# Kernel optimization log

Hardware: AMD Instinct MI355X
Metric: run time of the kernel (lower is better)

Reference implementation:

```python
import jax, jax.numpy as jnp
from jax import lax
import numpy as np

BLOCK_SIZE = 11   # cv2 blockSize (odd)
CONSTANT = 2.0    # cv2 C
MAXVAL = 255.0


def _box_mean(x, k):
    """Local k x k mean with BORDER_REPLICATE, matching cv2 ADAPTIVE_THRESH_MEAN_C.
    x: [N,H,W,1] float32. Separable 1-D box filters for efficiency."""
    pad = k // 2
    xp = jnp.pad(x, ((0, 0), (pad, pad), (pad, pad), (0, 0)), mode='edge')
    kh = jnp.full((k, 1, 1, 1), 1.0 / k, dtype=x.dtype)  # HWIO
    kw = jnp.full((1, k, 1, 1), 1.0 / k, dtype=x.dtype)
    dn = ('NHWC', 'HWIO', 'NHWC')
    y = lax.conv_general_dilated(xp, kh, (1, 1), 'VALID', dimension_numbers=dn)
    y = lax.conv_general_dilated(y, kw, (1, 1), 'VALID', dimension_numbers=dn)
    return y  # [N,H,W,1]


def setup_inputs() -> dict:
    key = jax.random.key(0)
    # grayscale pixel intensities in [0, 255]
    x = jax.random.uniform(key, (128, 512, 512, 1), dtype=jnp.float32) * 255.0
    return {"x": x}


def reference(x):
    # cv2.adaptiveThreshold(..., ADAPTIVE_THRESH_MEAN_C, THRESH_BINARY_INV, blockSize, C):
    #   T(x,y) = mean_{kxk}(src) - C
    #   dst = 0 if src > T else maxValue
    thresh = _box_mean(x, BLOCK_SIZE) - CONSTANT
    out = jnp.where(x > thresh, jnp.float32(0.0), jnp.float32(MAXVAL))
    return out
```

## Files before the change

kernel.cpp:

```cpp
#include <hip/hip_runtime.h>


constexpr int W   = 512;
constexpr int H   = 512;
constexpr int PAD = 5;
constexpr int KS  = 11;
constexpr int TPB = 256;
constexpr int RPB = 32;
constexpr int WP  = W + 2 * PAD;

__global__ __launch_bounds__(TPB, 8)
void AdaptiveThresholding_57904749085171_kernel(const float* __restrict__ x,
                                                float* __restrict__ out)
{
    __shared__ float mv[2][WP];

    const int t  = (int)threadIdx.x;
    const int c0 = 2 * t;
    const int y0 = (int)blockIdx.x * RPB;
    const size_t ioff = (size_t)blockIdx.y * (size_t)(W * H);
    const float* __restrict__ xi = x + ioff;
    float* __restrict__ oi = out + ioff;
    const float wv = (float)(1.0 / 11.0);

    float r0[KS], r1[KS];

    #pragma unroll
    for (int k = 0; k < KS - 1; ++k) {
        int j = y0 - PAD + k;
        int src = j < 0 ? 0 : (j >= H ? H - 1 : j);
        const float2 v = *(const float2*)(xi + (size_t)src * W + c0);
        r0[k] = v.x; r1[k] = v.y;
    }
    float p0, p1;
    {
        int j = y0 + PAD;
        int src = j >= H ? H - 1 : j;
        const float2 v = *(const float2*)(xi + (size_t)src * W + c0);
        p0 = v.x; p1 = v.y;
    }

    for (int y = y0; y < y0 + RPB; ++y) {
        r0[KS - 1] = p0;
        r1[KS - 1] = p1;

        float a0 = 0.0f, a1 = 0.0f;
        #pragma unroll
        for (int d = 0; d < KS; ++d) {
            a0 = fmaf(r0[d], wv, a0);
            a1 = fmaf(r1[d], wv, a1);
        }

        const int pp = (y - y0) & 1;
        mv[pp][PAD + c0]     = a0;
        mv[pp][PAD + c0 + 1] = a1;
        if (t == 0) {
            #pragma unroll
            for (int i = 0; i < PAD; ++i) mv[pp][i] = a0;
        } else if (t == TPB - 1) {
            #pragma unroll
            for (int i = 0; i < PAD; ++i) mv[pp][W + PAD + i] = a1;
        }

        const float xv0 = r0[PAD];
        const float xv1 = r1[PAD];

        if (y + 1 < y0 + RPB) {
            int j = y + 1 + PAD;
            int src = j >= H ? H - 1 : j;
            const float2 v = *(const float2*)(xi + (size_t)src * W + c0);
            p0 = v.x; p1 = v.y;
        }

        #pragma unroll
        for (int d = 0; d < KS - 1; ++d) {
            r0[d] = r0[d + 1];
            r1[d] = r1[d + 1];
        }

        __syncthreads();

        float m0 = 0.0f, m1 = 0.0f;
        #pragma unroll
        for (int e = 0; e < KS; ++e) m0 = fmaf(mv[pp][c0 + e], wv, m0);
        #pragma unroll
        for (int e = 0; e < KS; ++e) m1 = fmaf(mv[pp][c0 + 1 + e], wv, m1);

        float2 o;
        o.x = (xv0 > m0 - 2.0f) ? 0.0f : 255.0f;
        o.y = (xv1 > m1 - 2.0f) ? 0.0f : 255.0f;
        *(float2*)(oi + (size_t)y * W + c0) = o;
    }
}

extern "C" void kernel_launch(void* const* d_in, const int* in_sizes, int n_in,
                              void* d_out, int out_size, void* d_ws, size_t ws_size,
                              hipStream_t stream)
{
    const float* x = (const float*)d_in[0];
    float* out = (float*)d_out;
    const int n_imgs = in_sizes[0] / (W * H);

    dim3 grid(H / RPB, n_imgs);
    dim3 block(TPB);
    AdaptiveThresholding_57904749085171_kernel<<<grid, block, 0, stream>>>(x, out);
}
```

Baseline: 52.79 us.

## Use single-wavefront blocks with warp shuffles for horizontal box pass

Result: slower. 95.70 us (+81.3%).

```diff
diff --git a/kernel.cpp b/kernel.cpp
--- a/kernel.cpp
+++ b/kernel.cpp
@@ -5,91 +5,92 @@
 constexpr int H   = 512;
 constexpr int PAD = 5;
 constexpr int KS  = 11;
-constexpr int TPB = 256;
-constexpr int RPB = 32;
-constexpr int WP  = W + 2 * PAD;
+constexpr int CPT = 8;
+constexpr int TPB = 64;
+constexpr int RPB = 16;
+constexpr int STRIPS = H / RPB;
 
-__global__ __launch_bounds__(TPB, 8)
+typedef float f32x4 __attribute__((ext_vector_type(4)));
+
+__global__ __launch_bounds__(TPB)
 void AdaptiveThresholding_57904749085171_kernel(const float* __restrict__ x,
                                                 float* __restrict__ out)
 {
-    __shared__ float mv[2][WP];
-
-    const int t  = (int)threadIdx.x;
-    const int c0 = 2 * t;
-    const int y0 = (int)blockIdx.x * RPB;
-    const size_t ioff = (size_t)blockIdx.y * (size_t)(W * H);
+    const int l     = (int)threadIdx.x;
+    const int strip = (int)blockIdx.x;
+    const int img   = strip / STRIPS;
+    const int y0    = (strip % STRIPS) * RPB;
+    const size_t ioff = (size_t)img * (size_t)(W * H);
     const float* __restrict__ xi = x + ioff;
     float* __restrict__ oi = out + ioff;
+    const int cbase = l * CPT;
     const float wv = (float)(1.0 / 11.0);
 
-    float r0[KS], r1[KS];
+    float ring[KS][CPT];
 
     #pragma unroll
-    for (int k = 0; k < KS - 1; ++k) {
-        int j = y0 - PAD + k;
-        int src = j < 0 ? 0 : (j >= H ? H - 1 : j);
-        const float2 v = *(const float2*)(xi + (size_t)src * W + c0);
-        r0[k] = v.x; r1[k] = v.y;
-    }
-    float p0, p1;
-    {
-        int j = y0 + PAD;
-        int src = j >= H ? H - 1 : j;
-        const float2 v = *(const float2*)(xi + (size_t)src * W + c0);
-        p0 = v.x; p1 = v.y;
+    for (int j = 0; j < KS - 1; ++j) {
+        int row = y0 - PAD + j;
+        row = row < 0 ? 0 : (row >= H ? H - 1 : row);
+        const f32x4* p = (const f32x4*)(xi + (size_t)row * W + cbase);
+        const f32x4 a = p[0], b = p[1];
+        #pragma unroll
+        for (int i = 0; i < 4; ++i) { ring[j][i] = a[i]; ring[j][4 + i] = b[i]; }
     }
 
-    for (int y = y0; y < y0 + RPB; ++y) {
-        r0[KS - 1] = p0;
-        r1[KS - 1] = p1;
-
-        float a0 = 0.0f, a1 = 0.0f;
-        #pragma unroll
-        for (int d = 0; d < KS; ++d) {
-            a0 = fmaf(r0[d], wv, a0);
-            a1 = fmaf(r1[d], wv, a1);
+    #pragma unroll
+    for (int k = 0; k < RPB; ++k) {
+        {
+            int row = y0 + PAD + k;
+            row = row >= H ? H - 1 : row;
+            const f32x4* p = (const f32x4*)(xi + (size_t)row * W + cbase);
+            const f32x4 a = p[0], b = p[1];
+            #pragma unroll
+            for (int i = 0; i < 4; ++i) {
+                ring[(10 + k) % KS][i]     = a[i];
+                ring[(10 + k) % KS][4 + i] = b[i];
+            }
         }
 
-        const int pp = (y - y0) & 1;
-        mv[pp][PAD + c0]     = a0;
-        mv[pp][PAD + c0 + 1] = a1;
-        if (t == 0) {
+        float a[CPT];
+        #pragma unroll
+        for (int i = 0; i < CPT; ++i) {
+            float s = 0.0f;
             #pragma unroll
-            for (int i = 0; i < PAD; ++i) mv[pp][i] = a0;
-        } else if (t == TPB - 1) {
-            #pragma unroll
-            for (int i = 0; i < PAD; ++i) mv[pp][W + PAD + i] = a1;
+            for (int d = 0; d < KS; ++d) s = fmaf(ring[(k + d) % KS][i], wv, s);
+            a[i] = s;
         }
 
-        const float xv0 = r0[PAD];
-        const float xv1 = r1[PAD];
-
-        if (y + 1 < y0 + RPB) {
-            int j = y + 1 + PAD;
-            int src = j >= H ? H - 1 : j;
-            const float2 v = *(const float2*)(xi + (size_t)src * W + c0);
-            p0 = v.x; p1 = v.y;
+        float z[CPT + 2 * PAD];
+        #pragma unroll
+        for (int q = 0; q < PAD; ++q) {
+            const float vL = __shfl(a[3 + q], l - 1, 64);
+            z[q] = (l == 0) ? a[0] : vL;
+        }
+        #pragma unroll
+        for (int i = 0; i < CPT; ++i) z[PAD + i] = a[i];
+        #pragma unroll
+        for (int q = 0; q < PAD; ++q) {
+            const float vR = __shfl(a[q], l + 1, 64);
+            z[PAD + CPT + q] = (l == 63) ? a[7] : vR;
         }
 
+        float o[CPT];
         #pragma unroll
-        for (int d = 0; d < KS - 1; ++d) {
-            r0[d] = r0[d + 1];
-            r1[d] = r1[d + 1];
+        for (int i = 0; i < CPT; ++i) {
+            float m = 0.0f;
+            #pragma unroll
+            for (int d = 0; d < KS; ++d) m = fmaf(z[i + d], wv, m);
+            const float xv = ring[(k + PAD) % KS][i];
+            o[i] = (xv > m - 2.0f) ? 0.0f : 255.0f;
         }
 
-        __syncthreads();
-
-        float m0 = 0.0f, m1 = 0.0f;
+        f32x4 o0, o1;
         #pragma unroll
-        for (int e = 0; e < KS; ++e) m0 = fmaf(mv[pp][c0 + e], wv, m0);
-        #pragma unroll
-        for (int e = 0; e < KS; ++e) m1 = fmaf(mv[pp][c0 + 1 + e], wv, m1);
-
-        float2 o;
-        o.x = (xv0 > m0 - 2.0f) ? 0.0f : 255.0f;
-        o.y = (xv1 > m1 - 2.0f) ? 0.0f : 255.0f;
-        *(float2*)(oi + (size_t)y * W + c0) = o;
+        for (int i = 0; i < 4; ++i) { o0[i] = o[i]; o1[i] = o[4 + i]; }
+        f32x4* op = (f32x4*)(oi + (size_t)(y0 + k) * W + cbase);
+        __builtin_nontemporal_store(o0, op);
+        __builtin_nontemporal_store(o1, op + 1);
     }
 }
 
@@ -101,7 +102,7 @@
     float* out = (float*)d_out;
     const int n_imgs = in_sizes[0] / (W * H);
 
-    dim3 grid(H / RPB, n_imgs);
+    dim3 grid(n_imgs * STRIPS);
     dim3 block(TPB);
     AdaptiveThresholding_57904749085171_kernel<<<grid, block, 0, stream>>>(x, out);
 }
```

## Process two rows per barrier with 4-wide columns and bank-strided shared layout

Applied to the files above, without the earlier changes.

Measured after the change: 60.29 us. 14.2% more time.

```diff
diff --git a/kernel.cpp b/kernel.cpp
--- a/kernel.cpp
+++ b/kernel.cpp
@@ -5,91 +5,118 @@
 constexpr int H   = 512;
 constexpr int PAD = 5;
 constexpr int KS  = 11;
-constexpr int TPB = 256;
+constexpr int TPB = 128;
 constexpr int RPB = 32;
-constexpr int WP  = W + 2 * PAD;
+constexpr int NPH = RPB / 2;
 
-__global__ __launch_bounds__(TPB, 8)
+typedef float f32x4 __attribute__((ext_vector_type(4)));
+
+__global__ __launch_bounds__(TPB)
 void AdaptiveThresholding_57904749085171_kernel(const float* __restrict__ x,
                                                 float* __restrict__ out)
 {
-    __shared__ float mv[2][WP];
+    __shared__ float2 q[2][4][132];
 
     const int t  = (int)threadIdx.x;
-    const int c0 = 2 * t;
+    const int c0 = 4 * t;
     const int y0 = (int)blockIdx.x * RPB;
     const size_t ioff = (size_t)blockIdx.y * (size_t)(W * H);
     const float* __restrict__ xi = x + ioff;
     float* __restrict__ oi = out + ioff;
     const float wv = (float)(1.0 / 11.0);
 
-    float r0[KS], r1[KS];
+    float rr[12][4];
 
     #pragma unroll
-    for (int k = 0; k < KS - 1; ++k) {
-        int j = y0 - PAD + k;
+    for (int d = 0; d < 10; ++d) {
+        int j = y0 - PAD + d;
         int src = j < 0 ? 0 : (j >= H ? H - 1 : j);
-        const float2 v = *(const float2*)(xi + (size_t)src * W + c0);
-        r0[k] = v.x; r1[k] = v.y;
+        const f32x4 v = *(const f32x4*)(xi + (size_t)src * W + c0);
+        #pragma unroll
+        for (int jj = 0; jj < 4; ++jj) rr[d][jj] = v[jj];
     }
-    float p0, p1;
+    f32x4 pa, pb;
     {
-        int j = y0 + PAD;
-        int src = j >= H ? H - 1 : j;
-        const float2 v = *(const float2*)(xi + (size_t)src * W + c0);
-        p0 = v.x; p1 = v.y;
+        int ja = y0 + 5;  int sa = ja >= H ? H - 1 : ja;
+        int jb = y0 + 6;  int sb = jb >= H ? H - 1 : jb;
+        pa = *(const f32x4*)(xi + (size_t)sa * W + c0);
+        pb = *(const f32x4*)(xi + (size_t)sb * W + c0);
     }
 
-    for (int y = y0; y < y0 + RPB; ++y) {
-        r0[KS - 1] = p0;
-        r1[KS - 1] = p1;
+    for (int k = 0; k < NPH; ++k) {
+        const int Y = y0 + 2 * k;
 
-        float a0 = 0.0f, a1 = 0.0f;
         #pragma unroll
-        for (int d = 0; d < KS; ++d) {
-            a0 = fmaf(r0[d], wv, a0);
-            a1 = fmaf(r1[d], wv, a1);
+        for (int jj = 0; jj < 4; ++jj) { rr[10][jj] = pa[jj]; rr[11][jj] = pb[jj]; }
+
+        if (k + 1 < NPH) {
+            int ja = Y + 7;  int sa = ja >= H ? H - 1 : ja;
+            int jb = Y + 8;  int sb = jb >= H ? H - 1 : jb;
+            pa = *(const f32x4*)(xi + (size_t)sa * W + c0);
+            pb = *(const f32x4*)(xi + (size_t)sb * W + c0);
         }
 
-        const int pp = (y - y0) & 1;
-        mv[pp][PAD + c0]     = a0;
-        mv[pp][PAD + c0 + 1] = a1;
-        if (t == 0) {
+        float aE[4], aO[4];
+        #pragma unroll
+        for (int jj = 0; jj < 4; ++jj) {
+            float s0 = 0.0f;
             #pragma unroll
-            for (int i = 0; i < PAD; ++i) mv[pp][i] = a0;
-        } else if (t == TPB - 1) {
+            for (int d = 0; d < KS; ++d) s0 = fmaf(rr[d][jj], wv, s0);
+            aE[jj] = s0;
+            float s1 = 0.0f;
             #pragma unroll
-            for (int i = 0; i < PAD; ++i) mv[pp][W + PAD + i] = a1;
+            for (int d = 1; d < KS + 1; ++d) s1 = fmaf(rr[d][jj], wv, s1);
+            aO[jj] = s1;
         }
 
-        const float xv0 = r0[PAD];
-        const float xv1 = r1[PAD];
-
-        if (y + 1 < y0 + RPB) {
-            int j = y + 1 + PAD;
-            int src = j >= H ? H - 1 : j;
-            const float2 v = *(const float2*)(xi + (size_t)src * W + c0);
-            p0 = v.x; p1 = v.y;
+        const int pp = k & 1;
+        q[pp][1][t + 1] = make_float2(aE[0], aO[0]);
+        q[pp][2][t + 1] = make_float2(aE[1], aO[1]);
+        q[pp][3][t + 1] = make_float2(aE[2], aO[2]);
+        q[pp][0][t + 2] = make_float2(aE[3], aO[3]);
+        if (t == 0) {
+            const float2 e = make_float2(aE[0], aO[0]);
+            q[pp][0][0] = e; q[pp][1][0] = e; q[pp][2][0] = e; q[pp][3][0] = e;
+            q[pp][0][1] = e;
+        } else if (t == TPB - 1) {
+            const float2 e = make_float2(aE[3], aO[3]);
+            q[pp][1][129] = e; q[pp][2][129] = e; q[pp][3][129] = e;
+            q[pp][0][130] = e; q[pp][1][130] = e;
         }
 
+        float xE[4], xO[4];
         #pragma unroll
-        for (int d = 0; d < KS - 1; ++d) {
-            r0[d] = r0[d + 1];
-            r1[d] = r1[d + 1];
-        }
+        for (int jj = 0; jj < 4; ++jj) { xE[jj] = rr[5][jj]; xO[jj] = rr[6][jj]; }
+
+        #pragma unroll
+        for (int d = 0; d < 10; ++d)
+            #pragma unroll
+            for (int jj = 0; jj < 4; ++jj) rr[d][jj] = rr[d + 2][jj];
 
         __syncthreads();
 
-        float m0 = 0.0f, m1 = 0.0f;
+        float mE[4] = {0.f, 0.f, 0.f, 0.f};
+        float mO[4] = {0.f, 0.f, 0.f, 0.f};
         #pragma unroll
-        for (int e = 0; e < KS; ++e) m0 = fmaf(mv[pp][c0 + e], wv, m0);
+        for (int m = 0; m < 14; ++m) {
+            const float2 v = q[pp][m & 3][t + (m >> 2)];
+            #pragma unroll
+            for (int jj = 0; jj < 4; ++jj) {
+                if (m >= jj && m <= jj + 10) {
+                    mE[jj] = fmaf(v.x, wv, mE[jj]);
+                    mO[jj] = fmaf(v.y, wv, mO[jj]);
+                }
+            }
+        }
+
+        f32x4 oE, oO;
         #pragma unroll
-        for (int e = 0; e < KS; ++e) m1 = fmaf(mv[pp][c0 + 1 + e], wv, m1);
-
-        float2 o;
-        o.x = (xv0 > m0 - 2.0f) ? 0.0f : 255.0f;
-        o.y = (xv1 > m1 - 2.0f) ? 0.0f : 255.0f;
-        *(float2*)(oi + (size_t)y * W + c0) = o;
+        for (int jj = 0; jj < 4; ++jj) {
+            oE[jj] = (xE[jj] > mE[jj] - 2.0f) ? 0.0f : 255.0f;
+            oO[jj] = (xO[jj] > mO[jj] - 2.0f) ? 0.0f : 255.0f;
+        }
+        *(f32x4*)(oi + (size_t)Y * W + c0)       = oE;
+        *(f32x4*)(oi + (size_t)(Y + 1) * W + c0) = oO;
     }
 }
 
```
